# Kernel tuning notes

Hardware: AMD Instinct MI355X
Metric: run time of the kernel (lower is better)

## Reference

```python
import jax, jax.numpy as jnp
import numpy as np


def _maxpool2x2(x):
    # x: [B, H, W, C] -> [B, H//2, W//2, C], VALID 2x2/2 max pool
    B, H, W, C = x.shape
    return x.reshape(B, H // 2, 2, W // 2, 2, C).max(axis=(2, 4))


def setup_inputs() -> dict:
    key = jax.random.key(0)
    ks = jax.random.split(key, 6)
    B, H, W, C = 16, 64, 64, 512
    x = jax.random.normal(ks[0], (B, H, W, C), dtype=jnp.float32)
    w_theta = jax.random.normal(ks[1], (C, C // 8), dtype=jnp.float32) * 0.02
    w_phi = jax.random.normal(ks[2], (C, C // 8), dtype=jnp.float32) * 0.02
    w_g = jax.random.normal(ks[3], (C, C // 2), dtype=jnp.float32) * 0.02
    w_o = jax.random.normal(ks[4], (C // 2, C), dtype=jnp.float32) * 0.02
    return {
        "x": x,
        "w_theta": w_theta, "b_theta": jnp.zeros((C // 8,), jnp.float32),
        "w_phi": w_phi, "b_phi": jnp.zeros((C // 8,), jnp.float32),
        "w_g": w_g, "b_g": jnp.zeros((C // 2,), jnp.float32),
        "w_o": w_o, "b_o": jnp.zeros((C,), jnp.float32),
        "sigma": jnp.ones((1,), jnp.float32) * 0.1,
    }


def reference(x, w_theta, b_theta, w_phi, b_phi, w_g, b_g, w_o, b_o, sigma):
    B, H, W, C = x.shape
    n_feat = H * W
    # 1x1 convs are channel-mixing GEMMs over pixels
    theta = (jnp.einsum('bhwc,cd->bhwd', x, w_theta) + b_theta).reshape(B, n_feat, C // 8)
    phi = _maxpool2x2(jnp.einsum('bhwc,cd->bhwd', x, w_phi) + b_phi).reshape(B, n_feat // 4, C // 8)
    g = _maxpool2x2(jnp.einsum('bhwc,cd->bhwd', x, w_g) + b_g).reshape(B, n_feat // 4, C // 2)
    # [B, HW, HW/4] attention (no scaling, matching SAGAN/tf source)
    attn = jax.nn.softmax(jnp.einsum('bqd,bkd->bqk', theta, phi), axis=-1)
    attn_g = jnp.einsum('bqk,bkd->bqd', attn, g).reshape(B, H, W, C // 2)
    attn_g = jnp.einsum('bhwd,dc->bhwc', attn_g, w_o) + b_o
    return x + sigma * attn_g
```

## Files before the change

### kernel.cpp

```cpp
#include <hip/hip_runtime.h>
#include <math.h>

#define NB    16
#define NPIX  4096
#define NPOOL 1024
#define CIN   512
#define CD    64
#define CG    256

typedef unsigned short u16;
typedef unsigned int   u32;
typedef __attribute__((ext_vector_type(8)))  u16    u16x8;
typedef __attribute__((ext_vector_type(8)))  __bf16 bf16x8;
typedef __attribute__((ext_vector_type(16))) float  f32x16;

__device__ __forceinline__ u16 f2bf(float x) {
    u32 u = __builtin_bit_cast(u32, x);
    u += 0x7fffu + ((u >> 16) & 1u);
    return (u16)(u >> 16);
}
__device__ __forceinline__ float bf2f(u16 h) {
    u32 u = ((u32)h) << 16;
    return __builtin_bit_cast(float, u);
}
__device__ __forceinline__ f32x16 mfma32(u16x8 a, u16x8 b, f32x16 c) {
    return __builtin_amdgcn_mfma_f32_32x32x16_bf16(
        __builtin_bit_cast(bf16x8, a), __builtin_bit_cast(bf16x8, b), c, 0, 0, 0);
}

__global__ __launch_bounds__(256) void prep_kernel(
    const float* __restrict__ wt, const float* __restrict__ wp,
    const float* __restrict__ wg, const float* __restrict__ wo,
    const float* __restrict__ bt, const float* __restrict__ bp,
    const float* __restrict__ bg,
    u16* __restrict__ WT, u16* __restrict__ WOT, float* __restrict__ biasP)
{
    const int bx = blockIdx.x;
    const int t  = threadIdx.x;

    if (bx == 320) {
        for (int i = t; i < 384; i += 256)
            biasP[i] = (i < 64) ? bt[i] : (i < 128) ? bp[i - 64] : bg[i - 128];
        return;
    }

    const float* src; u16* dst; int N, K, kt, nt;
    if (bx < 32)       { src = wt; dst = WT;             N = 64;  K = 512; kt = bx >> 1;        nt = bx & 1; }
    else if (bx < 64)  { src = wp; dst = WT + 64 * 512;  N = 64;  K = 512; kt = (bx - 32) >> 1; nt = (bx - 32) & 1; }
    else if (bx < 192) { src = wg; dst = WT + 128 * 512; N = 256; K = 512; kt = (bx - 64) >> 3; nt = (bx - 64) & 7; }
    else               { src = wo; dst = WOT;            N = 512; K = 256; kt = (bx - 192) >> 4; nt = (bx - 192) & 15; }

    __shared__ float tile[32][33];
    {
        int r  = t >> 3;
        int c4 = (t & 7) * 4;
        float4 v = *(const float4*)(src + (size_t)(kt * 32 + r) * N + nt * 32 + c4);
        tile[r][c4]     = v.x;
        tile[r][c4 + 1] = v.y;
        tile[r][c4 + 2] = v.z;
        tile[r][c4 + 3] = v.w;
    }
    __syncthreads();
    {
        int n  = t >> 3;
        int k4 = (t & 7) * 4;
        ushort4 wv;
        wv.x = f2bf(tile[k4][n]);
        wv.y = f2bf(tile[k4 + 1][n]);
        wv.z = f2bf(tile[k4 + 2][n]);
        wv.w = f2bf(tile[k4 + 3][n]);
        *(ushort4*)(dst + (size_t)(nt * 32 + n) * K + kt * 32 + k4) = wv;
    }
}

#define AST 40
__global__ __launch_bounds__(256) void proj_gemm_kernel(
    const float* __restrict__ x, const u16* __restrict__ WT,
    const float* __restrict__ biasP,
    u16* __restrict__ theta, u16* __restrict__ phiF, u16* __restrict__ gF)
{
    __shared__ u16 As[128 * AST];
    __shared__ u16 Bs[128 * AST];

    const int t  = threadIdx.x;
    const int w  = t >> 6, l = t & 63, lr = l & 31, lh = l >> 5;
    const int sb = (blockIdx.x & 7) * 192 + (blockIdx.x >> 3);
    const int mt = sb / 3, nt = sb % 3;
    const int m0 = mt * 128, n0 = nt * 128;
    const int mw = (w & 1) * 64, nw = (w >> 1) * 64;

    const int arow = t >> 3;
    const int ac4  = (t & 7) * 4;
    const int brow = t >> 2;
    const int bc8  = (t & 3) * 8;

    f32x16 acc[2][2] = {};

    for (int k0 = 0; k0 < 512; k0 += 32) {
#pragma unroll
        for (int i = 0; i < 4; ++i) {
            const int r = i * 32 + arow;
            float4 v = *(const float4*)(x + (size_t)(m0 + r) * 512 + k0 + ac4);
            ushort4 wv;
            wv.x = f2bf(v.x); wv.y = f2bf(v.y); wv.z = f2bf(v.z); wv.w = f2bf(v.w);
            *(ushort4*)&As[r * AST + ac4] = wv;
        }
#pragma unroll
        for (int i = 0; i < 2; ++i) {
            const int r = i * 64 + brow;
            u16x8 v = *(const u16x8*)(WT + (size_t)(n0 + r) * 512 + k0 + bc8);
            *(u16x8*)&Bs[r * AST + bc8] = v;
        }
        __syncthreads();
#pragma unroll
        for (int ki = 0; ki < 2; ++ki) {
            u16x8 af0 = *(const u16x8*)&As[(mw + lr)      * AST + ki * 16 + lh * 8];
            u16x8 af1 = *(const u16x8*)&As[(mw + 32 + lr) * AST + ki * 16 + lh * 8];
            u16x8 bf0 = *(const u16x8*)&Bs[(nw + lr)      * AST + ki * 16 + lh * 8];
            u16x8 bf1 = *(const u16x8*)&Bs[(nw + 32 + lr) * AST + ki * 16 + lh * 8];
            acc[0][0] = mfma32(af0, bf0, acc[0][0]);
            acc[0][1] = mfma32(af0, bf1, acc[0][1]);
            acc[1][0] = mfma32(af1, bf0, acc[1][0]);
            acc[1][1] = mfma32(af1, bf1, acc[1][1]);
        }
        __syncthreads();
    }

#pragma unroll
    for (int mi = 0; mi < 2; ++mi) {
#pragma unroll
        for (int ni = 0; ni < 2; ++ni) {
            const int nb = n0 + nw + ni * 32;
            const int n  = nb + lr;
            const float bv = biasP[n];
            u16* dst; int ld, col;
            if (nb < 64)        { dst = theta; ld = 64;  col = n; }
            else if (nb < 128)  { dst = phiF;  ld = 64;  col = n - 64; }
            else                { dst = gF;    ld = 256; col = n - 128; }
#pragma unroll
            for (int r = 0; r < 16; ++r) {
                int row = m0 + mw + mi * 32 + (r & 3) + 8 * (r >> 2) + 4 * lh;
                dst[(size_t)row * ld + col] = f2bf(acc[mi][ni][r] + bv);
            }
        }
    }
}

__global__ __launch_bounds__(256) void pool_kernel(
    const u16* __restrict__ phiF, const u16* __restrict__ gF,
    u16* __restrict__ phif, u16* __restrict__ gtf)
{
    const int t  = threadIdx.x;
    const int b  = blockIdx.x >> 5;
    const int ph = blockIdx.x & 31;

    {
        const int pw = t >> 3, dq = (t & 7) * 8;
        const u16* base = phiF + ((size_t)(b * NPIX + 2 * ph * 64 + 2 * pw)) * 64 + dq;
        u16x8 v00 = *(const u16x8*)(base);
        u16x8 v01 = *(const u16x8*)(base + 64);
        u16x8 v10 = *(const u16x8*)(base + 64 * 64);
        u16x8 v11 = *(const u16x8*)(base + 64 * 64 + 64);
        u16x8 m;
#pragma unroll
        for (int j = 0; j < 8; ++j) {
            float mf = fmaxf(fmaxf(bf2f(v00[j]), bf2f(v01[j])),
                             fmaxf(bf2f(v10[j]), bf2f(v11[j])));
            m[j] = f2bf(mf);
        }
        const int ki = dq >> 4, lhw = (dq >> 3) & 1;
        *(u16x8*)(phif + (((size_t)(b * 32 + ph) * 4 + ki) * 64 + (pw * 2 + lhw)) * 8) = m;
    }
    {
        const u16* gb = gF + ((size_t)(b * NPIX + 2 * ph * 64)) * 256 + t;
        u16 buf[32];
#pragma unroll
        for (int kp = 0; kp < 32; ++kp) {
            float m = fmaxf(
                fmaxf(bf2f(gb[(size_t)(2 * kp) * 256]),      bf2f(gb[(size_t)(2 * kp + 1) * 256])),
                fmaxf(bf2f(gb[(size_t)(64 + 2 * kp) * 256]), bf2f(gb[(size_t)(64 + 2 * kp + 1) * 256])));
            buf[kp] = f2bf(m);
        }
        const int db = t >> 5, lr = t & 31;
        u16* go = gtf + (((size_t)(b * 32 + ph) * 8 + db) * 2) * 512;
#pragma unroll
        for (int h = 0; h < 2; ++h)
#pragma unroll
            for (int lhw = 0; lhw < 2; ++lhw)
                *(u16x8*)(go + h * 512 + (lr * 2 + lhw) * 8) =
                    *(const u16x8*)&buf[h * 16 + lhw * 8];
    }
}

#define SLD 1032
__global__ __launch_bounds__(512) void attn_mfma_kernel(
    const u16* __restrict__ theta, const u16* __restrict__ phif,
    const u16* __restrict__ gtf, u16* __restrict__ attn_g)
{
    __shared__ u16   S[64 * SLD];
    __shared__ float rinv[64];

    const int t  = threadIdx.x;
    const int w  = t >> 6;
    const int l  = t & 63;
    const int lr = l & 31;
    const int lh = l >> 5;
    const int lslot = (lr * 2 + lh) * 8;
    const int sb = (blockIdx.x & 7) * 128 + (blockIdx.x >> 3);
    const int b  = sb >> 6;
    const int q0 = (sb & 63) * 64;

    const u16* thb0 = theta + ((size_t)(b * NPIX + q0 + lr)) * CD + lh * 8;
    const u16* thb1 = thb0 + (size_t)32 * CD;
    u16x8 af0[4], af1[4];
#pragma unroll
    for (int ki = 0; ki < 4; ++ki) {
        af0[ki] = *(const u16x8*)(thb0 + ki * 16);
        af1[ki] = *(const u16x8*)(thb1 + ki * 16);
    }

#pragma unroll 2
    for (int nt = 0; nt < 4; ++nt) {
        const int kb = w * 4 + nt;
        const int k0 = kb * 32;
        const u16* pb = phif + ((size_t)(b * 32 + kb) * 4) * 512 + lslot;
        u16x8 pf0 = *(const u16x8*)(pb);
        u16x8 pf1 = *(const u16x8*)(pb + 512);
        u16x8 pf2 = *(const u16x8*)(pb + 1024);
        u16x8 pf3 = *(const u16x8*)(pb + 1536);
        f32x16 acc0 = {}, acc1 = {};
        acc0 = mfma32(af0[0], pf0, acc0);  acc1 = mfma32(af1[0], pf0, acc1);
        acc0 = mfma32(af0[1], pf1, acc0);  acc1 = mfma32(af1[1], pf1, acc1);
        acc0 = mfma32(af0[2], pf2, acc0);  acc1 = mfma32(af1[2], pf2, acc1);
        acc0 = mfma32(af0[3], pf3, acc0);  acc1 = mfma32(af1[3], pf3, acc1);
#pragma unroll
        for (int r = 0; r < 16; ++r) {
            int row = (r & 3) + 8 * (r >> 2) + 4 * lh;
            S[row * SLD + k0 + lr]        = f2bf(acc0[r]);
            S[(32 + row) * SLD + k0 + lr] = f2bf(acc1[r]);
        }
    }
    __syncthreads();

    {
        const int row = t >> 3, cg = t & 7;
        u16* srow = S + row * SLD;
        float mx = -1e30f;
#pragma unroll
        for (int i = 0; i < 16; ++i) {
            u16x8 v = *(const u16x8*)(srow + cg * 8 + 64 * i);
#pragma unroll
            for (int j = 0; j < 8; ++j) mx = fmaxf(mx, bf2f(v[j]));
        }
        mx = fmaxf(mx, __shfl_xor(mx, 1));
        mx = fmaxf(mx, __shfl_xor(mx, 2));
        mx = fmaxf(mx, __shfl_xor(mx, 4));
        float sum = 0.f;
#pragma unroll
        for (int i = 0; i < 16; ++i) {
            u16* p = srow + cg * 8 + 64 * i;
            u16x8 v = *(const u16x8*)p;
            u16x8 e;
#pragma unroll
            for (int j = 0; j < 8; ++j) {
                float ev = __expf(bf2f(v[j]) - mx);
                sum += ev;
                e[j] = f2bf(ev);
            }
            *(u16x8*)p = e;
        }
        sum += __shfl_xor(sum, 1);
        sum += __shfl_xor(sum, 2);
        sum += __shfl_xor(sum, 4);
        if (cg == 0) rinv[row] = 1.0f / sum;
    }
    __syncthreads();

    const u16* gfb = gtf + ((size_t)(b * 32) * 16 + (size_t)w * 2) * 512 + lslot;
    const u16* ar0 = S + lr * SLD;
    const u16* ar1 = S + (32 + lr) * SLD;
    f32x16 o0a = {}, o0b = {}, o1a = {}, o1b = {};
#pragma unroll 4
    for (int kb = 0; kb < 32; ++kb) {
        const u16* gpk = gfb + (size_t)kb * (16 * 512);
        u16x8 b0  = *(const u16x8*)(gpk);
        u16x8 b1  = *(const u16x8*)(gpk + 512);
        const int k0 = kb * 32;
        u16x8 a00 = *(const u16x8*)(ar0 + k0 + lh * 8);
        u16x8 a01 = *(const u16x8*)(ar0 + k0 + 16 + lh * 8);
        u16x8 a10 = *(const u16x8*)(ar1 + k0 + lh * 8);
        u16x8 a11 = *(const u16x8*)(ar1 + k0 + 16 + lh * 8);
        o0a = mfma32(a00, b0, o0a);
        o0b = mfma32(a01, b1, o0b);
        o1a = mfma32(a10, b0, o1a);
        o1b = mfma32(a11, b1, o1b);
    }

    u16* obp = attn_g + ((size_t)(b * NPIX + q0)) * CG;
#pragma unroll
    for (int r = 0; r < 16; ++r) {
        int qrow = (r & 3) + 8 * (r >> 2) + 4 * lh;
        float inv0 = rinv[qrow];
        float inv1 = rinv[32 + qrow];
        obp[(size_t)qrow * CG + w * 32 + lr]        = f2bf((o0a[r] + o0b[r]) * inv0);
        obp[(size_t)(32 + qrow) * CG + w * 32 + lr] = f2bf((o1a[r] + o1b[r]) * inv1);
    }
}

__global__ __launch_bounds__(256) void out_gemm_kernel(
    const u16* __restrict__ attn_gB, const u16* __restrict__ WOT,
    const float* __restrict__ x, const float* __restrict__ bo,
    const float* __restrict__ sigma, float* __restrict__ out)
{
    __shared__ u16 As[128 * AST];
    __shared__ u16 Bs[128 * AST];

    const int t  = threadIdx.x;
    const int w  = t >> 6, l = t & 63, lr = l & 31, lh = l >> 5;
    const int sb = (blockIdx.x & 7) * 256 + (blockIdx.x >> 3);
    const int mt = sb >> 2, nt = sb & 3;
    const int m0 = mt * 128, n0 = nt * 128;
    const int mw = (w & 1) * 64, nw = (w >> 1) * 64;

    const int srow = t >> 2;
    const int sc8  = (t & 3) * 8;

    f32x16 acc[2][2] = {};

    for (int k0 = 0; k0 < 256; k0 += 32) {
#pragma unroll
        for (int i = 0; i < 2; ++i) {
            const int r = i * 64 + srow;
            u16x8 av = *(const u16x8*)(attn_gB + (size_t)(m0 + r) * 256 + k0 + sc8);
            *(u16x8*)&As[r * AST + sc8] = av;
            u16x8 bv = *(const u16x8*)(WOT + (size_t)(n0 + r) * 256 + k0 + sc8);
            *(u16x8*)&Bs[r * AST + sc8] = bv;
        }
        __syncthreads();
#pragma unroll
        for (int ki = 0; ki < 2; ++ki) {
            u16x8 af0 = *(const u16x8*)&As[(mw + lr)      * AST + ki * 16 + lh * 8];
            u16x8 af1 = *(const u16x8*)&As[(mw + 32 + lr) * AST + ki * 16 + lh * 8];
            u16x8 bf0 = *(const u16x8*)&Bs[(nw + lr)      * AST + ki * 16 + lh * 8];
            u16x8 bf1 = *(const u16x8*)&Bs[(nw + 32 + lr) * AST + ki * 16 + lh * 8];
            acc[0][0] = mfma32(af0, bf0, acc[0][0]);
            acc[0][1] = mfma32(af0, bf1, acc[0][1]);
            acc[1][0] = mfma32(af1, bf0, acc[1][0]);
            acc[1][1] = mfma32(af1, bf1, acc[1][1]);
        }
        __syncthreads();
    }

    const float s = sigma[0];
#pragma unroll
    for (int mi = 0; mi < 2; ++mi) {
#pragma unroll
        for (int ni = 0; ni < 2; ++ni) {
            const int n  = n0 + nw + ni * 32 + lr;
            const float bv = bo[n];
#pragma unroll
            for (int r = 0; r < 16; ++r) {
                int row = m0 + mw + mi * 32 + (r & 3) + 8 * (r >> 2) + 4 * lh;
                size_t idx = (size_t)row * 512 + n;
                out[idx] = x[idx] + s * (acc[mi][ni][r] + bv);
            }
        }
    }
}

extern "C" void kernel_launch(void* const* d_in, const int* in_sizes, int n_in,
                              void* d_out, int out_size, void* d_ws, size_t ws_size,
                              hipStream_t stream)
{
    const float* x     = (const float*)d_in[0];
    const float* wt    = (const float*)d_in[1];
    const float* bt    = (const float*)d_in[2];
    const float* wp    = (const float*)d_in[3];
    const float* bp    = (const float*)d_in[4];
    const float* wg    = (const float*)d_in[5];
    const float* bg    = (const float*)d_in[6];
    const float* wo    = (const float*)d_in[7];
    const float* bo    = (const float*)d_in[8];
    const float* sigma = (const float*)d_in[9];
    float* out = (float*)d_out;

    char* ws = (char*)d_ws;
    u16*   theta   = (u16*)(ws);
    u16*   phif    = (u16*)(ws + ((size_t)8  << 20));
    u16*   phiF    = (u16*)(ws + ((size_t)10 << 20));
    u16*   gF      = (u16*)(ws + ((size_t)18 << 20));
    u16*   attn_gB = (u16*)(ws + ((size_t)10 << 20));
    u16*   gtf     = (u16*)(ws + ((size_t)50 << 20));
    u16*   WT      = (u16*)(ws + ((size_t)58 << 20));
    u16*   WOT     = (u16*)(ws + ((size_t)58 << 20) + (384 << 10));
    float* biasP   = (float*)(ws + ((size_t)58 << 20) + (640 << 10));

    prep_kernel<<<321, 256, 0, stream>>>(wt, wp, wg, wo, bt, bp, bg, WT, WOT, biasP);
    proj_gemm_kernel<<<512 * 3, 256, 0, stream>>>(x, WT, biasP, theta, phiF, gF);
    pool_kernel<<<NB * 32, 256, 0, stream>>>(phiF, gF, phif, gtf);
    attn_mfma_kernel<<<NB * NPIX / 64, 512, 0, stream>>>(theta, phif, gtf, attn_gB);
    out_gemm_kernel<<<512 * 4, 256, 0, stream>>>(attn_gB, WOT, x, bo, sigma, out);
}
```

Measured before the change: 410.9 us.

## Double K-tile depth in projection/output GEMMs and software-prefetch g in attention

The projection and output GEMMs now stage 64-wide K slices in shared memory instead of 32, with the row stride padded to 72, which halves the number of barrier-separated loop iterations. The attention PV loop is manually unrolled into ping-pong register buffers that prefetch the next group of g fragments from global memory while MFMAs consume the current group. The aim is to cut barrier overhead and hide global load latency. In exchange, shared memory per block grows and register pressure rises from the prefetch buffers, which may lower occupancy.

After: 454.1 us. 1.11x slower.

```diff
diff --git a/kernel.cpp b/kernel.cpp
--- a/kernel.cpp
+++ b/kernel.cpp
@@ -73,7 +73,7 @@
     }
 }
 
-#define AST 40
+#define AST 72
 __global__ __launch_bounds__(256) void proj_gemm_kernel(
     const float* __restrict__ x, const u16* __restrict__ WT,
     const float* __restrict__ biasP,
@@ -89,31 +89,31 @@
     const int m0 = mt * 128, n0 = nt * 128;
     const int mw = (w & 1) * 64, nw = (w >> 1) * 64;
 
-    const int arow = t >> 3;
-    const int ac4  = (t & 7) * 4;
-    const int brow = t >> 2;
-    const int bc8  = (t & 3) * 8;
+    const int arow = t >> 4;
+    const int ac4  = (t & 15) * 4;
+    const int brow = t >> 3;
+    const int bc8  = (t & 7) * 8;
 
     f32x16 acc[2][2] = {};
 
-    for (int k0 = 0; k0 < 512; k0 += 32) {
-#pragma unroll
-        for (int i = 0; i < 4; ++i) {
-            const int r = i * 32 + arow;
+    for (int k0 = 0; k0 < 512; k0 += 64) {
+#pragma unroll
+        for (int i = 0; i < 8; ++i) {
+            const int r = i * 16 + arow;
             float4 v = *(const float4*)(x + (size_t)(m0 + r) * 512 + k0 + ac4);
             ushort4 wv;
             wv.x = f2bf(v.x); wv.y = f2bf(v.y); wv.z = f2bf(v.z); wv.w = f2bf(v.w);
             *(ushort4*)&As[r * AST + ac4] = wv;
         }
 #pragma unroll
-        for (int i = 0; i < 2; ++i) {
-            const int r = i * 64 + brow;
+        for (int i = 0; i < 4; ++i) {
+            const int r = i * 32 + brow;
             u16x8 v = *(const u16x8*)(WT + (size_t)(n0 + r) * 512 + k0 + bc8);
             *(u16x8*)&Bs[r * AST + bc8] = v;
         }
         __syncthreads();
 #pragma unroll
-        for (int ki = 0; ki < 2; ++ki) {
+        for (int ki = 0; ki < 4; ++ki) {
             u16x8 af0 = *(const u16x8*)&As[(mw + lr)      * AST + ki * 16 + lh * 8];
             u16x8 af1 = *(const u16x8*)&As[(mw + 32 + lr) * AST + ki * 16 + lh * 8];
             u16x8 bf0 = *(const u16x8*)&Bs[(nw + lr)      * AST + ki * 16 + lh * 8];
@@ -280,20 +280,54 @@
     const u16* ar0 = S + lr * SLD;
     const u16* ar1 = S + (32 + lr) * SLD;
     f32x16 o0a = {}, o0b = {}, o1a = {}, o1b = {};
-#pragma unroll 4
-    for (int kb = 0; kb < 32; ++kb) {
-        const u16* gpk = gfb + (size_t)kb * (16 * 512);
-        u16x8 b0  = *(const u16x8*)(gpk);
-        u16x8 b1  = *(const u16x8*)(gpk + 512);
-        const int k0 = kb * 32;
-        u16x8 a00 = *(const u16x8*)(ar0 + k0 + lh * 8);
-        u16x8 a01 = *(const u16x8*)(ar0 + k0 + 16 + lh * 8);
-        u16x8 a10 = *(const u16x8*)(ar1 + k0 + lh * 8);
-        u16x8 a11 = *(const u16x8*)(ar1 + k0 + 16 + lh * 8);
-        o0a = mfma32(a00, b0, o0a);
-        o0b = mfma32(a01, b1, o0b);
-        o1a = mfma32(a10, b0, o1a);
-        o1b = mfma32(a11, b1, o1b);
+
+    u16x8 p0A[4], p1A[4], p0B[4], p1B[4];
+#pragma unroll
+    for (int i = 0; i < 4; ++i) {
+        const u16* gpk = gfb + (size_t)i * 8192;
+        p0A[i] = *(const u16x8*)gpk;
+        p1A[i] = *(const u16x8*)(gpk + 512);
+    }
+#pragma unroll
+    for (int gp = 0; gp < 4; ++gp) {
+#pragma unroll
+        for (int i = 0; i < 4; ++i) {
+            const u16* gpk = gfb + (size_t)((2 * gp + 1) * 4 + i) * 8192;
+            p0B[i] = *(const u16x8*)gpk;
+            p1B[i] = *(const u16x8*)(gpk + 512);
+        }
+#pragma unroll
+        for (int i = 0; i < 4; ++i) {
+            const int k0 = ((2 * gp) * 4 + i) * 32;
+            u16x8 a00 = *(const u16x8*)(ar0 + k0 + lh * 8);
+            u16x8 a01 = *(const u16x8*)(ar0 + k0 + 16 + lh * 8);
+            u16x8 a10 = *(const u16x8*)(ar1 + k0 + lh * 8);
+            u16x8 a11 = *(const u16x8*)(ar1 + k0 + 16 + lh * 8);
+            o0a = mfma32(a00, p0A[i], o0a);
+            o0b = mfma32(a01, p1A[i], o0b);
+            o1a = mfma32(a10, p0A[i], o1a);
+            o1b = mfma32(a11, p1A[i], o1b);
+        }
+        if (gp < 3) {
+#pragma unroll
+            for (int i = 0; i < 4; ++i) {
+                const u16* gpk = gfb + (size_t)((2 * gp + 2) * 4 + i) * 8192;
+                p0A[i] = *(const u16x8*)gpk;
+                p1A[i] = *(const u16x8*)(gpk + 512);
+            }
+        }
+#pragma unroll
+        for (int i = 0; i < 4; ++i) {
+            const int k0 = ((2 * gp + 1) * 4 + i) * 32;
+            u16x8 a00 = *(const u16x8*)(ar0 + k0 + lh * 8);
+            u16x8 a01 = *(const u16x8*)(ar0 + k0 + 16 + lh * 8);
+            u16x8 a10 = *(const u16x8*)(ar1 + k0 + lh * 8);
+            u16x8 a11 = *(const u16x8*)(ar1 + k0 + 16 + lh * 8);
+            o0a = mfma32(a00, p0B[i], o0a);
+            o0b = mfma32(a01, p1B[i], o0b);
+            o1a = mfma32(a10, p0B[i], o1a);
+            o1b = mfma32(a11, p1B[i], o1b);
+        }
     }
 
     u16* obp = attn_g + ((size_t)(b * NPIX + q0)) * CG;
@@ -322,15 +356,15 @@
     const int m0 = mt * 128, n0 = nt * 128;
     const int mw = (w & 1) * 64, nw = (w >> 1) * 64;
 
-    const int srow = t >> 2;
-    const int sc8  = (t & 3) * 8;
+    const int srow = t >> 3;
+    const int sc8  = (t & 7) * 8;
 
     f32x16 acc[2][2] = {};
 
-    for (int k0 = 0; k0 < 256; k0 += 32) {
-#pragma unroll
-        for (int i = 0; i < 2; ++i) {
-            const int r = i * 64 + srow;
+    for (int k0 = 0; k0 < 256; k0 += 64) {
+#pragma unroll
+        for (int i = 0; i < 4; ++i) {
+            const int r = i * 32 + srow;
             u16x8 av = *(const u16x8*)(attn_gB + (size_t)(m0 + r) * 256 + k0 + sc8);
             *(u16x8*)&As[r * AST + sc8] = av;
             u16x8 bv = *(const u16x8*)(WOT + (size_t)(n0 + r) * 256 + k0 + sc8);
@@ -338,7 +372,7 @@
         }
         __syncthreads();
 #pragma unroll
-        for (int ki = 0; ki < 2; ++ki) {
+        for (int ki = 0; ki < 4; ++ki) {
             u16x8 af0 = *(const u16x8*)&As[(mw + lr)      * AST + ki * 16 + lh * 8];
             u16x8 af1 = *(const u16x8*)&As[(mw + 32 + lr) * AST + ki * 16 + lh * 8];
             u16x8 bf0 = *(const u16x8*)&Bs[(nw + lr)      * AST + ki * 16 + lh * 8];
```
